# Optimization experiments

Measured on AMD Instinct MI355X. Metric: run time of the kernel, lower is better.

The kernel has to match this reference:

```python
import jax, jax.numpy as jnp
import numpy as np

EPS = 1e-7  # tf.keras.backend.epsilon()
R_ITER = 3

def squash(v, axis=-1):
    # Eq.(1): scale = |s|^2 / (1+|s|^2) / |s|
    s2 = jnp.sum(v * v, axis=axis, keepdims=True)
    scale = s2 / (1.0 + s2) / jnp.sqrt(s2 + EPS)
    return scale * v

def setup_inputs() -> dict:
    key = jax.random.key(0)
    k1, k2 = jax.random.split(key)
    B, Ni, Di = 64, 1152, 8
    No, Do = 64, 16
    inputs = jax.random.normal(k1, (B, Ni, Di), dtype=jnp.float32)
    # W init: tf.random.normal(stddev=0.1)
    W = 0.1 * jax.random.normal(k2, (1, Ni, No, Do, Di), dtype=jnp.float32)
    return {"inputs": inputs, "W": W}

def reference(inputs, W):
    B, Ni, Di = inputs.shape
    No, Do = W.shape[2], W.shape[3]
    # inputs_hat[b,i,o,d] = W[i,o,d,k] @ inputs[b,i,k]  (tile+matmul fused)
    u_hat = jnp.einsum('iodk,bik->biod', W[0], inputs)  # [B,Ni,No,Do]
    # raw routing logits start at shape [1,Ni,No]; broadcast to [B,...] on first update
    b_logits = jnp.zeros((1, Ni, No), dtype=inputs.dtype)
    for it in range(R_ITER):
        c = jax.nn.softmax(b_logits, axis=2)            # over output caps
        s = jnp.sum(c[..., None] * u_hat, axis=1, keepdims=True)  # [B,1,No,Do]
        v = squash(s, axis=-1)                          # [B,1,No,Do]
        if it < R_ITER - 1:
            # agreement: <u_hat, v> over capsule dim
            b_logits = b_logits + jnp.sum(u_hat * v, axis=-1)  # [B,Ni,No]
    out = jnp.squeeze(v, axis=1)                        # [B,No,Do]
    routing_weights = c[..., None, None]                # [B,Ni,No,1,1] as in TF
    return out, routing_weights
```

## Files before the change

### kernel.cpp

```cpp
#include <hip/hip_runtime.h>


#define B_      64
#define NI_     1152
#define DI_     8
#define NO_     64
#define DO_     16
#define NOD_    1024
#define CH_     96
#define CI_     12
#define BG_     8
#define BSPLIT_ 8
#define V_ELEMS 65536
#define PADR    33

static_assert(CH_ * CI_ == NI_, "chunking");
static_assert(BG_ * BSPLIT_ == B_, "b split");

template <int MODE>
__global__ __launch_bounds__(256, 3)
void caps_pass(const float* __restrict__ X,
               const float* __restrict__ W,
               const float* __restrict__ vin,
               float* __restrict__ part,
               float* __restrict__ rw)
{
    __shared__ float  x_lds[BG_][CI_ * DI_];
    __shared__ float4 wtile[NO_ * PADR];
    __shared__ float  e_lds[BG_][NO_];
    __shared__ float  invS[BG_];

    const int t  = threadIdx.x;
    const int o  = t >> 2, q = t & 3;
    const int ch = blockIdx.x;
    const int b0 = blockIdx.y * BG_;
    const int i0 = ch * CI_;

    for (int f = t; f < BG_ * CI_ * DI_ / 4; f += 256) {
        int bb = f / (CI_ * DI_ / 4), r = f - bb * (CI_ * DI_ / 4);
        ((float4*)x_lds)[f] =
            ((const float4*)(X + ((size_t)(b0 + bb) * NI_ + i0) * DI_))[r];
    }
    float vreg[BG_][4];
    if (MODE >= 1) {
#pragma unroll
        for (int b = 0; b < BG_; ++b) {
            float4 qv = *((const float4*)(vin + (size_t)(b0 + b) * NOD_ + 4 * t));
            vreg[b][0]=qv.x; vreg[b][1]=qv.y; vreg[b][2]=qv.z; vreg[b][3]=qv.w;
        }
    }
    __syncthreads();

    float acc[BG_][4];
#pragma unroll
    for (int b = 0; b < BG_; ++b) { acc[b][0]=0.f; acc[b][1]=0.f; acc[b][2]=0.f; acc[b][3]=0.f; }

    const float4* Wq = (const float4*)W;

    for (int ci = 0; ci < CI_; ++ci) {
        const int i = i0 + ci;

        const float4* wg = Wq + (size_t)i * 2048;
        float4 tmp[8];
#pragma unroll
        for (int j = 0; j < 8; ++j) tmp[j] = wg[t + 256 * j];
#pragma unroll
        for (int j = 0; j < 8; ++j) {
            const int f = t + 256 * j;
            wtile[(f >> 5) * PADR + (f & 31)] = tmp[j];
        }
        __syncthreads();

        float wf[4][8];
#pragma unroll
        for (int jj = 0; jj < 4; ++jj) {
            float4 a0 = wtile[o * PADR + (4 * q + jj) * 2];
            float4 a1 = wtile[o * PADR + (4 * q + jj) * 2 + 1];
            wf[jj][0]=a0.x; wf[jj][1]=a0.y; wf[jj][2]=a0.z; wf[jj][3]=a0.w;
            wf[jj][4]=a1.x; wf[jj][5]=a1.y; wf[jj][6]=a1.z; wf[jj][7]=a1.w;
        }

        float u[BG_][4];
#pragma unroll
        for (int b = 0; b < BG_; ++b) {
            const float* xb = &x_lds[b][ci * DI_];
            const float x0=xb[0],x1=xb[1],x2=xb[2],x3=xb[3];
            const float x4=xb[4],x5=xb[5],x6=xb[6],x7=xb[7];
#pragma unroll
            for (int jj = 0; jj < 4; ++jj) {
                float s = wf[jj][0] * x0;
                s = fmaf(wf[jj][1], x1, s); s = fmaf(wf[jj][2], x2, s);
                s = fmaf(wf[jj][3], x3, s); s = fmaf(wf[jj][4], x4, s);
                s = fmaf(wf[jj][5], x5, s); s = fmaf(wf[jj][6], x6, s);
                s = fmaf(wf[jj][7], x7, s);
                u[b][jj] = s;
            }
            if (MODE >= 1) {
                float a = u[b][0]*vreg[b][0] + u[b][1]*vreg[b][1]
                        + u[b][2]*vreg[b][2] + u[b][3]*vreg[b][3];
                a += __shfl_xor(a, 1);
                a += __shfl_xor(a, 2);
                if (q == 0) e_lds[b][o] = __expf(a);
            } else {
                acc[b][0]+=u[b][0]; acc[b][1]+=u[b][1];
                acc[b][2]+=u[b][2]; acc[b][3]+=u[b][3];
            }
        }

        if (MODE >= 1) {
            __syncthreads();
            {
                const int bb = t >> 5, l = t & 31;
                float s = e_lds[bb][l] + e_lds[bb][l + 32];
                s += __shfl_xor(s, 1);  s += __shfl_xor(s, 2);  s += __shfl_xor(s, 4);
                s += __shfl_xor(s, 8);  s += __shfl_xor(s, 16);
                if (l == 0) invS[bb] = 1.0f / s;
            }
            __syncthreads();
#pragma unroll
            for (int b = 0; b < BG_; ++b) {
                const float c = e_lds[b][o] * invS[b];
                acc[b][0] = fmaf(c, u[b][0], acc[b][0]);
                acc[b][1] = fmaf(c, u[b][1], acc[b][1]);
                acc[b][2] = fmaf(c, u[b][2], acc[b][2]);
                acc[b][3] = fmaf(c, u[b][3], acc[b][3]);
                if (MODE == 2 && q == 0)
                    rw[((size_t)(b0 + b) * NI_ + i) * NO_ + o] = c;
            }
        } else {
            __syncthreads();
        }
    }

#pragma unroll
    for (int b = 0; b < BG_; ++b) {
        float4 val;
        val.x=acc[b][0]; val.y=acc[b][1]; val.z=acc[b][2]; val.w=acc[b][3];
        *((float4*)(part + (((size_t)(b0 + b) * CH_ + ch) * NOD_ + 4 * t))) = val;
    }
}

template <int MODE>
__global__ __launch_bounds__(128)
void caps_squash(const float* __restrict__ part, const float* __restrict__ v0in,
                 float* __restrict__ vout)
{
    const int c4 = blockIdx.x * 128 + threadIdx.x;
    const int b = c4 >> 8, od4 = c4 & 255;
    const float4* p = (const float4*)part + (size_t)b * CH_ * 256 + od4;
    float4 s = {0.f, 0.f, 0.f, 0.f};
#pragma unroll 8
    for (int ch = 0; ch < CH_; ++ch) {
        float4 q = p[(size_t)ch * 256];
        s.x += q.x; s.y += q.y; s.z += q.z; s.w += q.w;
    }
    if (MODE == 0) { s.x*=(1.f/64.f); s.y*=(1.f/64.f); s.z*=(1.f/64.f); s.w*=(1.f/64.f); }
    float s2 = s.x*s.x + s.y*s.y + s.z*s.z + s.w*s.w;
    s2 += __shfl_xor(s2, 1); s2 += __shfl_xor(s2, 2);
    const float scale = s2 / ((1.0f + s2) * sqrtf(s2 + 1e-7f));
    float4 v; v.x = scale*s.x; v.y = scale*s.y; v.z = scale*s.z; v.w = scale*s.w;
    if (MODE == 1) {
        float4 v0 = ((const float4*)v0in)[c4];
        v.x += v0.x; v.y += v0.y; v.z += v0.z; v.w += v0.w;
    }
    ((float4*)vout)[c4] = v;
}

__global__ __launch_bounds__(1024, 1)
void caps_naive(const float* __restrict__ X, const float* __restrict__ W,
                float* __restrict__ outv, float* __restrict__ outc)
{
    __shared__ float xs[NI_ * DI_];
    __shared__ float agree[NO_];
    __shared__ float expo[NO_];
    __shared__ float s2sh[NO_];
    __shared__ float den;

    const int b = blockIdx.x, tid = threadIdx.x;
    const int o = tid >> 4, d = tid & 15;

    for (int f = tid; f < NI_ * DI_; f += 1024)
        xs[f] = X[(size_t)b * NI_ * DI_ + f];
    __syncthreads();

    float vprev = 0.f, v0 = 0.f, vout = 0.f;
    for (int phase = 0; phase < 3; ++phase) {
        float sacc = 0.f;
        for (int i = 0; i < NI_; ++i) {
            const float* wp = W + (size_t)i * 8192 + (size_t)tid * 8;
            const float* xp = xs + i * DI_;
            float u = 0.f;
#pragma unroll
            for (int k = 0; k < 8; ++k) u = fmaf(wp[k], xp[k], u);
            if (phase == 0) { sacc += u; continue; }
            if (d == 0) agree[o] = 0.f;
            __syncthreads();
            atomicAdd(&agree[o], u * vprev);
            __syncthreads();
            if (tid == 0) den = 0.f;
            __syncthreads();
            if (d == 0) { float e = __expf(agree[o]); expo[o] = e; atomicAdd(&den, e); }
            __syncthreads();
            float c = expo[o] / den;
            sacc = fmaf(c, u, sacc);
            if (phase == 2 && d == 0)
                outc[((size_t)b * NI_ + i) * NO_ + o] = c;
            __syncthreads();
        }
        if (phase == 0) sacc *= (1.0f / 64.0f);
        if (d == 0) s2sh[o] = 0.f;
        __syncthreads();
        atomicAdd(&s2sh[o], sacc * sacc);
        __syncthreads();
        const float s2 = s2sh[o];
        const float scale = s2 / ((1.0f + s2) * sqrtf(s2 + 1e-7f));
        const float vv = scale * sacc;
        if (phase == 0)      { v0 = vv; vprev = vv; }
        else if (phase == 1) { vprev = v0 + vv; }
        else                 { vout = vv; }
        __syncthreads();
    }
    outv[(size_t)b * (NO_ * DO_) + tid] = vout;
}

extern "C" void kernel_launch(void* const* d_in, const int* in_sizes, int n_in,
                              void* d_out, int out_size, void* d_ws, size_t ws_size,
                              hipStream_t stream)
{
    const float *X, *W;
    if (in_sizes[0] < in_sizes[1]) { X = (const float*)d_in[0]; W = (const float*)d_in[1]; }
    else                           { X = (const float*)d_in[1]; W = (const float*)d_in[0]; }

    float* out  = (float*)d_out;
    float* outv = out;
    float* outc = out + V_ELEMS;

    const size_t needBig = ((size_t)B_ * CH_ * NOD_ + 2 * (size_t)B_ * NOD_) * sizeof(float);
    if (ws_size < needBig) {
        caps_naive<<<B_, 1024, 0, stream>>>(X, W, outv, outc);
        return;
    }

    float* part = (float*)d_ws;
    float* v0   = part + (size_t)B_ * CH_ * NOD_;
    float* w01  = v0 + (size_t)B_ * NOD_;

    dim3 gP(CH_, BSPLIT_), blk(256), gS(128), blkS(128);
    caps_pass<0><<<gP, blk, 0, stream>>>(X, W, nullptr, part, nullptr);
    caps_squash<0><<<gS, blkS, 0, stream>>>(part, nullptr, v0);
    caps_pass<1><<<gP, blk, 0, stream>>>(X, W, v0, part, nullptr);
    caps_squash<1><<<gS, blkS, 0, stream>>>(part, v0, w01);
    caps_pass<2><<<gP, blk, 0, stream>>>(X, W, w01, part, outc);
    caps_squash<2><<<gS, blkS, 0, stream>>>(part, nullptr, outv);
}
```

Before: 246.0 us.

## Load W directly into registers with prefetch, drop LDS weight tile

Each thread now reads its own 32 weights for the next input capsule straight from global memory into registers, prefetching one iteration ahead, instead of staging the whole 32KB weight slice through padded shared memory. It also double-buffers the exp/inverse-sum shared arrays by iteration parity, which lets one barrier per iteration go, and removes all barriers in mode 0. The aim is to cut LDS traffic and synchronisation and to overlap the weight fetch with the FMA work. The global reads become strided per thread (128 bytes contiguous each) rather than fully coalesced float4 sweeps, which may cost some memory efficiency.

```diff
diff --git a/kernel.cpp b/kernel.cpp
--- a/kernel.cpp
+++ b/kernel.cpp
@@ -12,7 +12,6 @@
 #define BG_     8
 #define BSPLIT_ 8
 #define V_ELEMS 65536
-#define PADR    33
 
 static_assert(CH_ * CI_ == NI_, "chunking");
 static_assert(BG_ * BSPLIT_ == B_, "b split");
@@ -25,10 +24,9 @@
                float* __restrict__ part,
                float* __restrict__ rw)
 {
-    __shared__ float  x_lds[BG_][CI_ * DI_];
-    __shared__ float4 wtile[NO_ * PADR];
-    __shared__ float  e_lds[BG_][NO_];
-    __shared__ float  invS[BG_];
+    __shared__ float x_lds[BG_][CI_ * DI_];
+    __shared__ float e_lds[2][BG_][NO_];
+    __shared__ float invS[2][BG_];
 
     const int t  = threadIdx.x;
     const int o  = t >> 2, q = t & 3;
@@ -36,11 +34,23 @@
     const int b0 = blockIdx.y * BG_;
     const int i0 = ch * CI_;
 
+    const float4* wp = (const float4*)W + (size_t)i0 * 2048 + t * 8;
+
+    float wf[4][8];
+#pragma unroll
+    for (int jj = 0; jj < 4; ++jj) {
+        float4 a0 = wp[2 * jj], a1 = wp[2 * jj + 1];
+        wf[jj][0]=a0.x; wf[jj][1]=a0.y; wf[jj][2]=a0.z; wf[jj][3]=a0.w;
+        wf[jj][4]=a1.x; wf[jj][5]=a1.y; wf[jj][6]=a1.z; wf[jj][7]=a1.w;
+    }
+    wp += 2048;
+
     for (int f = t; f < BG_ * CI_ * DI_ / 4; f += 256) {
         int bb = f / (CI_ * DI_ / 4), r = f - bb * (CI_ * DI_ / 4);
         ((float4*)x_lds)[f] =
             ((const float4*)(X + ((size_t)(b0 + bb) * NI_ + i0) * DI_))[r];
     }
+
     float vreg[BG_][4];
     if (MODE >= 1) {
 #pragma unroll
@@ -49,36 +59,16 @@
             vreg[b][0]=qv.x; vreg[b][1]=qv.y; vreg[b][2]=qv.z; vreg[b][3]=qv.w;
         }
     }
+
+    float acc[BG_][4];
+#pragma unroll
+    for (int b = 0; b < BG_; ++b) { acc[b][0]=0.f; acc[b][1]=0.f; acc[b][2]=0.f; acc[b][3]=0.f; }
+
     __syncthreads();
 
-    float acc[BG_][4];
-#pragma unroll
-    for (int b = 0; b < BG_; ++b) { acc[b][0]=0.f; acc[b][1]=0.f; acc[b][2]=0.f; acc[b][3]=0.f; }
-
-    const float4* Wq = (const float4*)W;
-
     for (int ci = 0; ci < CI_; ++ci) {
-        const int i = i0 + ci;
-
-        const float4* wg = Wq + (size_t)i * 2048;
-        float4 tmp[8];
-#pragma unroll
-        for (int j = 0; j < 8; ++j) tmp[j] = wg[t + 256 * j];
-#pragma unroll
-        for (int j = 0; j < 8; ++j) {
-            const int f = t + 256 * j;
-            wtile[(f >> 5) * PADR + (f & 31)] = tmp[j];
-        }
-        __syncthreads();
-
-        float wf[4][8];
-#pragma unroll
-        for (int jj = 0; jj < 4; ++jj) {
-            float4 a0 = wtile[o * PADR + (4 * q + jj) * 2];
-            float4 a1 = wtile[o * PADR + (4 * q + jj) * 2 + 1];
-            wf[jj][0]=a0.x; wf[jj][1]=a0.y; wf[jj][2]=a0.z; wf[jj][3]=a0.w;
-            wf[jj][4]=a1.x; wf[jj][5]=a1.y; wf[jj][6]=a1.z; wf[jj][7]=a1.w;
-        }
+        const int i   = i0 + ci;
+        const int par = ci & 1;
 
         float u[BG_][4];
 #pragma unroll
@@ -100,26 +90,36 @@
                         + u[b][2]*vreg[b][2] + u[b][3]*vreg[b][3];
                 a += __shfl_xor(a, 1);
                 a += __shfl_xor(a, 2);
-                if (q == 0) e_lds[b][o] = __expf(a);
+                if (q == 0) e_lds[par][b][o] = __expf(a);
             } else {
                 acc[b][0]+=u[b][0]; acc[b][1]+=u[b][1];
                 acc[b][2]+=u[b][2]; acc[b][3]+=u[b][3];
             }
         }
 
+        if (ci + 1 < CI_) {
+#pragma unroll
+            for (int jj = 0; jj < 4; ++jj) {
+                float4 a0 = wp[2 * jj], a1 = wp[2 * jj + 1];
+                wf[jj][0]=a0.x; wf[jj][1]=a0.y; wf[jj][2]=a0.z; wf[jj][3]=a0.w;
+                wf[jj][4]=a1.x; wf[jj][5]=a1.y; wf[jj][6]=a1.z; wf[jj][7]=a1.w;
+            }
+            wp += 2048;
+        }
+
         if (MODE >= 1) {
             __syncthreads();
             {
                 const int bb = t >> 5, l = t & 31;
-                float s = e_lds[bb][l] + e_lds[bb][l + 32];
+                float s = e_lds[par][bb][l] + e_lds[par][bb][l + 32];
                 s += __shfl_xor(s, 1);  s += __shfl_xor(s, 2);  s += __shfl_xor(s, 4);
                 s += __shfl_xor(s, 8);  s += __shfl_xor(s, 16);
-                if (l == 0) invS[bb] = 1.0f / s;
+                if (l == 0) invS[par][bb] = 1.0f / s;
             }
             __syncthreads();
 #pragma unroll
             for (int b = 0; b < BG_; ++b) {
-                const float c = e_lds[b][o] * invS[b];
+                const float c = e_lds[par][b][o] * invS[par][b];
                 acc[b][0] = fmaf(c, u[b][0], acc[b][0]);
                 acc[b][1] = fmaf(c, u[b][1], acc[b][1]);
                 acc[b][2] = fmaf(c, u[b][2], acc[b][2]);
@@ -127,8 +127,6 @@
                 if (MODE == 2 && q == 0)
                     rw[((size_t)(b0 + b) * NI_ + i) * NO_ + o] = c;
             }
-        } else {
-            __syncthreads();
         }
     }
 
```

Result: slower. 255.9 us (+4.0%).
